# Kernel tuning notes

Hardware: AMD Instinct MI355X
Metric: run time of the kernel (lower is better)

The kernel has to match this reference:

```python
import jax, jax.numpy as jnp
import numpy as np

N, E, DIN, DH, DOUT, G, H = 40000, 400000, 256, 128, 128, 256, 4
BN_EPS = 1e-5      # nn.BatchNorm1d default
SM_EPS = 1e-16     # PyG softmax eps
NEG_SLOPE = 0.2    # GATConv default negative_slope


def _gat(x, src, dst, W, a_src, a_dst, b, heads, out_ch):
    # x:[N,Fin] W:[Fin,heads*out_ch] a_*:[heads,out_ch] b:[out_ch]
    n = x.shape[0]
    h = (x @ W).reshape(n, heads, out_ch)                     # [N,H,C]
    e = (h * a_src).sum(-1)[src] + (h * a_dst).sum(-1)[dst]   # [E,H] attention logits
    e = jnp.where(e > 0, e, NEG_SLOPE * e)                    # leaky_relu
    m = jax.ops.segment_max(e, dst, num_segments=n)           # segment softmax over incoming edges
    p = jnp.exp(e - m[dst])
    z = jax.ops.segment_sum(p, dst, num_segments=n)
    alpha = p / (z[dst] + SM_EPS)                             # [E,H]
    out = jax.ops.segment_sum(h[src] * alpha[:, :, None], dst, num_segments=n)  # [N,H,C]
    return out.mean(axis=1) + b                               # concat=False -> mean over heads, then bias


def _bn(x, g, b, m, v):
    # eval-mode BatchNorm1d with running stats
    return (x - m) * jax.lax.rsqrt(v + BN_EPS) * g + b


def setup_inputs():
    key = jax.random.key(0)
    ks = jax.random.split(key, 16)
    def rn(k, shape, fan):
        return jax.random.normal(k, shape, jnp.float32) / np.sqrt(fan).astype(np.float32)
    return {
        "x": jax.random.normal(ks[0], (N, DIN), jnp.float32),
        "src": jax.random.randint(ks[1], (E,), 0, N),
        "dst": jax.random.randint(ks[2], (E,), 0, N),
        "batch": jnp.sort(jax.random.randint(ks[3], (N,), 0, G)),
        "W1": rn(ks[4], (DIN, H * DH), DIN), "as1": rn(ks[5], (H, DH), DH), "ad1": rn(ks[6], (H, DH), DH), "b1": jnp.zeros((DH,), jnp.float32),
        "g1": jnp.ones((DH,), jnp.float32), "be1": jnp.zeros((DH,), jnp.float32), "m1": jnp.zeros((DH,), jnp.float32), "v1": jnp.ones((DH,), jnp.float32),
        "W2": rn(ks[7], (DH, H * DH), DH), "as2": rn(ks[8], (H, DH), DH), "ad2": rn(ks[9], (H, DH), DH), "b2": jnp.zeros((DH,), jnp.float32),
        "g2": jnp.ones((DH,), jnp.float32), "be2": jnp.zeros((DH,), jnp.float32), "m2": jnp.zeros((DH,), jnp.float32), "v2": jnp.ones((DH,), jnp.float32),
        "W3": rn(ks[10], (DH, DOUT), DH), "as3": rn(ks[11], (1, DOUT), DOUT), "ad3": rn(ks[12], (1, DOUT), DOUT), "b3": jnp.zeros((DOUT,), jnp.float32),
    }


def reference(x, src, dst, batch, W1, as1, ad1, b1, g1, be1, m1, v1,
              W2, as2, ad2, b2, g2, be2, m2, v2, W3, as3, ad3, b3):
    n = x.shape[0]
    loop = jnp.arange(n)
    s = jnp.concatenate([src, loop])  # PyG GATConv add_self_loops=True
    d = jnp.concatenate([dst, loop])
    h = jax.nn.elu(_gat(x, s, d, W1, as1, ad1, b1, H, DH))
    h = _bn(h, g1, be1, m1, v1)
    h = jax.nn.elu(_gat(h, s, d, W2, as2, ad2, b2, H, DH))
    h = _bn(h, g2, be2, m2, v2)
    h = _gat(h, s, d, W3, as3, ad3, b3, 1, DOUT)
    tot = jax.ops.segment_sum(h, batch, num_segments=G)      # global_mean_pool
    cnt = jax.ops.segment_sum(jnp.ones((n,), h.dtype), batch, num_segments=G)
    return tot / jnp.maximum(cnt, 1.0)[:, None]
```

## Files before the change

kernel.cpp:

```cpp
#include <hip/hip_runtime.h>
#include <cstdint>

#define N_NODES 40000
#define N_EDGES 400000
#define DIN 256
#define DHID 128
#define NG 256
#define NHEAD 4
#define ETOT (N_EDGES + N_NODES)

typedef __attribute__((ext_vector_type(8))) short short8;
typedef __attribute__((ext_vector_type(8))) unsigned short bfx8;
typedef __attribute__((ext_vector_type(4))) unsigned short bfx4;
typedef __attribute__((ext_vector_type(4))) float floatx4;

static __device__ __forceinline__ unsigned short f2bf(float f) {
    unsigned u = __float_as_uint(f);
    unsigned r = (u + 0x7FFFu + ((u >> 16) & 1u)) >> 16;
    return (unsigned short)r;
}
static __device__ __forceinline__ float bf2f(unsigned short s) {
    return __uint_as_float((unsigned)s << 16);
}


__global__ void count_kernel(const int* __restrict__ dst, int* __restrict__ deg) {
    int i = blockIdx.x * 256 + threadIdx.x;
    if (i >= ETOT) return;
    int d = (i < N_EDGES) ? dst[i] : (i - N_EDGES);
    atomicAdd(&deg[d], 1);
}

__global__ __launch_bounds__(1024) void scan_kernel(const int* __restrict__ deg,
                                                    int* __restrict__ offs,
                                                    int* __restrict__ cursor) {
    const int VPT = 40;
    __shared__ int wsum[16];
    int t = threadIdx.x;
    int lane = t & 63, wv = t >> 6;
    int base = t * VPT;
    int vals[VPT];
    int run = 0;
#pragma unroll
    for (int i = 0; i < VPT; i++) {
        int idx = base + i;
        int v = (idx < N_NODES) ? deg[idx] : 0;
        vals[i] = run;
        run += v;
    }
    int inc = run;
#pragma unroll
    for (int off = 1; off < 64; off <<= 1) {
        int n = __shfl_up(inc, off, 64);
        if (lane >= off) inc += n;
    }
    if (lane == 63) wsum[wv] = inc;
    __syncthreads();
    if (t == 0) {
        int c = 0;
#pragma unroll
        for (int i = 0; i < 16; i++) { int v = wsum[i]; wsum[i] = c; c += v; }
    }
    __syncthreads();
    int excl = wsum[wv] + inc - run;
#pragma unroll
    for (int i = 0; i < VPT; i++) {
        int idx = base + i;
        if (idx < N_NODES) { int o = excl + vals[i]; offs[idx] = o; cursor[idx] = o; }
    }
    if (t == 0) offs[N_NODES] = ETOT;
}

__global__ void fill_kernel(const int* __restrict__ src, const int* __restrict__ dst,
                            int* __restrict__ cursor, int* __restrict__ csr,
                            int* __restrict__ dstp) {
    int i = blockIdx.x * 256 + threadIdx.x;
    if (i >= ETOT) return;
    int s, d;
    if (i < N_EDGES) { s = src[i]; d = dst[i]; } else { s = d = i - N_EDGES; }
    int pos = atomicAdd(&cursor[d], 1);
    csr[pos] = s;
    dstp[pos] = d;
}


__global__ void cvt_bf16_kernel(const float* __restrict__ in, unsigned short* __restrict__ out,
                                int n) {
    int i = blockIdx.x * 256 + threadIdx.x;
    if (i >= n) return;
    out[i] = f2bf(in[i]);
}

__global__ void transpose_w_kernel(const float* __restrict__ W, unsigned short* __restrict__ Wt,
                                   int K, int Nn) {
    int i = blockIdx.x * 256 + threadIdx.x;
    if (i >= K * Nn) return;
    int k = i / Nn, n = i - k * Nn;
    Wt[(size_t)n * K + k] = f2bf(W[i]);
}


template <int K, int NCOL>
__global__ __launch_bounds__(256) void mfma_gemm_kernel(const unsigned short* __restrict__ A,
                                                        const unsigned short* __restrict__ Bt,
                                                        unsigned short* __restrict__ C,
                                                        const float* __restrict__ asrc,
                                                        const float* __restrict__ adst,
                                                        float* __restrict__ ssrc,
                                                        float* __restrict__ sdst) {
    constexpr int KC = 128;
    constexpr int KP = KC + 8;
    constexpr int SH = NCOL / 128;
    __shared__ alignas(16) unsigned short A_lds[64][KP];
    __shared__ alignas(16) unsigned short B_lds[128][KP];

    const int tid = threadIdx.x;
    const int lane = tid & 63, wave = tid >> 6;
    const int row0 = blockIdx.x * 64;
    const int head = blockIdx.y;
    const int col0 = head * 128;
    const int cq = lane & 15, rq = lane >> 4;

    floatx4 acc[4][2] = {};

    for (int k0 = 0; k0 < K; k0 += KC) {
        if (k0) __syncthreads();
#pragma unroll
        for (int r = 0; r < 4; r++) {
            int i = r * 256 + tid;
            int row = i >> 4, slot = i & 15;
            short8 v = *(const short8*)(A + (size_t)(row0 + row) * K + k0 + slot * 8);
            *(short8*)&A_lds[row][slot * 8] = v;
        }
#pragma unroll
        for (int r = 0; r < 8; r++) {
            int i = r * 256 + tid;
            int col = i >> 4, slot = i & 15;
            short8 v = *(const short8*)(Bt + (size_t)(col0 + col) * K + k0 + slot * 8);
            *(short8*)&B_lds[col][slot * 8] = v;
        }
        __syncthreads();

#pragma unroll
        for (int kk = 0; kk < KC; kk += 32) {
            short8 af[4], bfr[2];
#pragma unroll
            for (int i = 0; i < 4; i++)
                af[i] = *(const short8*)&A_lds[i * 16 + cq][kk + rq * 8];
#pragma unroll
            for (int j = 0; j < 2; j++)
                bfr[j] = *(const short8*)&B_lds[wave * 32 + j * 16 + cq][kk + rq * 8];
#pragma unroll
            for (int i = 0; i < 4; i++)
#pragma unroll
                for (int j = 0; j < 2; j++)
                    acc[i][j] = __builtin_amdgcn_mfma_f32_16x16x32_bf16(af[i], bfr[j], acc[i][j], 0, 0, 0);
        }
    }

#pragma unroll
    for (int i = 0; i < 4; i++)
#pragma unroll
        for (int j = 0; j < 2; j++) {
            unsigned short* cp = C + (size_t)(row0 + i * 16 + rq * 4) * NCOL + col0 + wave * 32 + j * 16 + cq;
#pragma unroll
            for (int r = 0; r < 4; r++)
                cp[(size_t)r * NCOL] = f2bf(acc[i][j][r]);
        }

    const float* ah = asrc + head * 128;
    const float* dh = adst + head * 128;
    float a0 = ah[wave * 32 + cq], a1 = ah[wave * 32 + 16 + cq];
    float d0 = dh[wave * 32 + cq], d1 = dh[wave * 32 + 16 + cq];

    __syncthreads();
    float* sred = (float*)&A_lds[0][0];
    float* dred = sred + 256;

#pragma unroll
    for (int i = 0; i < 4; i++)
#pragma unroll
        for (int r = 0; r < 4; r++) {
            float ss = acc[i][0][r] * a0 + acc[i][1][r] * a1;
            float sd = acc[i][0][r] * d0 + acc[i][1][r] * d1;
#pragma unroll
            for (int m = 1; m <= 8; m <<= 1) {
                ss += __shfl_xor(ss, m, 64);
                sd += __shfl_xor(sd, m, 64);
            }
            if (cq == 0) {
                int row = i * 16 + rq * 4 + r;
                sred[wave * 64 + row] = ss;
                dred[wave * 64 + row] = sd;
            }
        }
    __syncthreads();
    if (tid < 64) {
        float ss = sred[tid] + sred[64 + tid] + sred[128 + tid] + sred[192 + tid];
        float sd = dred[tid] + dred[64 + tid] + dred[128 + tid] + dred[192 + tid];
        ssrc[(size_t)(row0 + tid) * SH + head] = ss;
        sdst[(size_t)(row0 + tid) * SH + head] = sd;
    }
}


__global__ void edge_alpha4_kernel(const int* __restrict__ csr, const int* __restrict__ dstp,
                                   const float4* __restrict__ ssrc4,
                                   const float4* __restrict__ sdst4,
                                   float4* __restrict__ elog4) {
    int p = blockIdx.x * 256 + threadIdx.x;
    if (p >= ETOT) return;
    int s = csr[p], d = dstp[p];
    float4 es = ssrc4[s], ed = sdst4[d];
    float4 e;
    e.x = es.x + ed.x; e.x = e.x > 0.f ? e.x : 0.2f * e.x;
    e.y = es.y + ed.y; e.y = e.y > 0.f ? e.y : 0.2f * e.y;
    e.z = es.z + ed.z; e.z = e.z > 0.f ? e.z : 0.2f * e.z;
    e.w = es.w + ed.w; e.w = e.w > 0.f ? e.w : 0.2f * e.w;
    elog4[p] = e;
}

__global__ void edge_alpha1_kernel(const int* __restrict__ csr, const int* __restrict__ dstp,
                                   const float* __restrict__ ssrc1,
                                   const float* __restrict__ sdst1,
                                   float* __restrict__ elog1) {
    int p = blockIdx.x * 256 + threadIdx.x;
    if (p >= ETOT) return;
    int s = csr[p], d = dstp[p];
    float e = ssrc1[s] + sdst1[d];
    e = e > 0.f ? e : 0.2f * e;
    elog1[p] = e;
}


__global__ __launch_bounds__(256) void agg4_kernel(const int* __restrict__ offs,
                                                   const int* __restrict__ csr,
                                                   const unsigned short* __restrict__ hbuf,
                                                   const float4* __restrict__ elog4,
                                                   const float* __restrict__ bias,
                                                   const float* __restrict__ bng,
                                                   const float* __restrict__ bnb,
                                                   const float* __restrict__ bnm,
                                                   const float* __restrict__ bnv,
                                                   unsigned short* __restrict__ outb) {
    int wave = threadIdx.x >> 6, lane = threadIdx.x & 63;
    int d = blockIdx.x * 4 + wave;
    int off = offs[d];
    int deg = offs[d + 1] - off;
    int hh = lane >> 4;
    float acc[8] = {};

    if (deg <= 64) {
        float4 ev; int sreg = 0;
        if (lane < deg) { ev = elog4[off + lane]; sreg = csr[off + lane]; }
        else { ev.x = ev.y = ev.z = ev.w = -1e30f; }
        float4 mx = ev;
#pragma unroll
        for (int m = 32; m >= 1; m >>= 1) {
            mx.x = fmaxf(mx.x, __shfl_xor(mx.x, m, 64));
            mx.y = fmaxf(mx.y, __shfl_xor(mx.y, m, 64));
            mx.z = fmaxf(mx.z, __shfl_xor(mx.z, m, 64));
            mx.w = fmaxf(mx.w, __shfl_xor(mx.w, m, 64));
        }
        float4 p;
        p.x = (lane < deg) ? __expf(ev.x - mx.x) : 0.f;
        p.y = (lane < deg) ? __expf(ev.y - mx.y) : 0.f;
        p.z = (lane < deg) ? __expf(ev.z - mx.z) : 0.f;
        p.w = (lane < deg) ? __expf(ev.w - mx.w) : 0.f;
        float4 z = p;
#pragma unroll
        for (int m = 32; m >= 1; m >>= 1) {
            z.x += __shfl_xor(z.x, m, 64);
            z.y += __shfl_xor(z.y, m, 64);
            z.z += __shfl_xor(z.z, m, 64);
            z.w += __shfl_xor(z.w, m, 64);
        }
        float4 alpha;
        alpha.x = p.x / (z.x + 1e-16f);
        alpha.y = p.y / (z.y + 1e-16f);
        alpha.z = p.z / (z.z + 1e-16f);
        alpha.w = p.w / (z.w + 1e-16f);

        for (int j = 0; j < deg; j++) {
            int s = __shfl(sreg, j, 64);
            float a0 = __shfl(alpha.x, j, 64);
            float a1 = __shfl(alpha.y, j, 64);
            float a2 = __shfl(alpha.z, j, 64);
            float a3 = __shfl(alpha.w, j, 64);
            float a = hh == 0 ? a0 : hh == 1 ? a1 : hh == 2 ? a2 : a3;
            bfx8 hv = *(const bfx8*)(hbuf + (size_t)s * 512 + lane * 8);
#pragma unroll
            for (int i = 0; i < 8; i++) acc[i] += a * bf2f(hv[i]);
        }
    } else {
        float4 mx; mx.x = mx.y = mx.z = mx.w = -1e30f;
        for (int j = lane; j < deg; j += 64) {
            float4 e = elog4[off + j];
            mx.x = fmaxf(mx.x, e.x); mx.y = fmaxf(mx.y, e.y);
            mx.z = fmaxf(mx.z, e.z); mx.w = fmaxf(mx.w, e.w);
        }
#pragma unroll
        for (int m = 32; m >= 1; m >>= 1) {
            mx.x = fmaxf(mx.x, __shfl_xor(mx.x, m, 64));
            mx.y = fmaxf(mx.y, __shfl_xor(mx.y, m, 64));
            mx.z = fmaxf(mx.z, __shfl_xor(mx.z, m, 64));
            mx.w = fmaxf(mx.w, __shfl_xor(mx.w, m, 64));
        }
        float4 z; z.x = z.y = z.z = z.w = 0.f;
        for (int j = lane; j < deg; j += 64) {
            float4 e = elog4[off + j];
            z.x += __expf(e.x - mx.x); z.y += __expf(e.y - mx.y);
            z.z += __expf(e.z - mx.z); z.w += __expf(e.w - mx.w);
        }
#pragma unroll
        for (int m = 32; m >= 1; m >>= 1) {
            z.x += __shfl_xor(z.x, m, 64);
            z.y += __shfl_xor(z.y, m, 64);
            z.z += __shfl_xor(z.z, m, 64);
            z.w += __shfl_xor(z.w, m, 64);
        }
        float4 inv;
        inv.x = 1.f / (z.x + 1e-16f); inv.y = 1.f / (z.y + 1e-16f);
        inv.z = 1.f / (z.z + 1e-16f); inv.w = 1.f / (z.w + 1e-16f);
        float mc = hh == 0 ? mx.x : hh == 1 ? mx.y : hh == 2 ? mx.z : mx.w;
        float ic = hh == 0 ? inv.x : hh == 1 ? inv.y : hh == 2 ? inv.z : inv.w;
        for (int j = 0; j < deg; j++) {
            float4 e = elog4[off + j];
            int s = csr[off + j];
            float ec = hh == 0 ? e.x : hh == 1 ? e.y : hh == 2 ? e.z : e.w;
            float a = __expf(ec - mc) * ic;
            bfx8 hv = *(const bfx8*)(hbuf + (size_t)s * 512 + lane * 8);
#pragma unroll
            for (int i = 0; i < 8; i++) acc[i] += a * bf2f(hv[i]);
        }
    }

#pragma unroll
    for (int i = 0; i < 8; i++) {
        acc[i] += __shfl_xor(acc[i], 16, 64);
        acc[i] += __shfl_xor(acc[i], 32, 64);
    }
    if (lane < 16) {
        int c0 = lane * 8;
        bfx8 o;
#pragma unroll
        for (int i = 0; i < 8; i++) {
            int c = c0 + i;
            float v = acc[i] * 0.25f + bias[c];
            v = v > 0.f ? v : (__expf(v) - 1.0f);
            float sc = bng[c] * rsqrtf(bnv[c] + 1e-5f);
            v = (v - bnm[c]) * sc + bnb[c];
            o[i] = f2bf(v);
        }
        *(bfx8*)(outb + (size_t)d * 128 + c0) = o;
    }
}


__global__ __launch_bounds__(256) void agg1_kernel(const int* __restrict__ offs,
                                                   const int* __restrict__ csr,
                                                   const unsigned short* __restrict__ hbuf1,
                                                   const float* __restrict__ elog1,
                                                   const float* __restrict__ bias,
                                                   float* __restrict__ h3out) {
    int wave = threadIdx.x >> 6, lane = threadIdx.x & 63;
    int d = blockIdx.x * 4 + wave;
    int off = offs[d];
    int deg = offs[d + 1] - off;
    int half = lane >> 5, li = lane & 31;
    float acc[4] = {};

    if (deg <= 64) {
        float ev = -1e30f; int sreg = 0;
        if (lane < deg) { ev = elog1[off + lane]; sreg = csr[off + lane]; }
        float mx = ev;
#pragma unroll
        for (int m = 32; m >= 1; m >>= 1) mx = fmaxf(mx, __shfl_xor(mx, m, 64));
        float p = (lane < deg) ? __expf(ev - mx) : 0.f;
        float z = p;
#pragma unroll
        for (int m = 32; m >= 1; m >>= 1) z += __shfl_xor(z, m, 64);
        float alpha = p / (z + 1e-16f);
        for (int j = half; j < deg; j += 2) {
            int s = __shfl(sreg, j, 64);
            float a = __shfl(alpha, j, 64);
            bfx4 hv = *(const bfx4*)(hbuf1 + (size_t)s * 128 + li * 4);
#pragma unroll
            for (int i = 0; i < 4; i++) acc[i] += a * bf2f(hv[i]);
        }
    } else {
        float mx = -1e30f;
        for (int j = lane; j < deg; j += 64) mx = fmaxf(mx, elog1[off + j]);
#pragma unroll
        for (int m = 32; m >= 1; m >>= 1) mx = fmaxf(mx, __shfl_xor(mx, m, 64));
        float z = 0.f;
        for (int j = lane; j < deg; j += 64) z += __expf(elog1[off + j] - mx);
#pragma unroll
        for (int m = 32; m >= 1; m >>= 1) z += __shfl_xor(z, m, 64);
        float inv = 1.f / (z + 1e-16f);
        for (int j = half; j < deg; j += 2) {
            int s = csr[off + j];
            float a = __expf(elog1[off + j] - mx) * inv;
            bfx4 hv = *(const bfx4*)(hbuf1 + (size_t)s * 128 + li * 4);
#pragma unroll
            for (int i = 0; i < 4; i++) acc[i] += a * bf2f(hv[i]);
        }
    }

#pragma unroll
    for (int i = 0; i < 4; i++) acc[i] += __shfl_xor(acc[i], 32, 64);
    if (lane < 32) {
        float4 o;
        o.x = acc[0] + bias[li * 4];
        o.y = acc[1] + bias[li * 4 + 1];
        o.z = acc[2] + bias[li * 4 + 2];
        o.w = acc[3] + bias[li * 4 + 3];
        *(float4*)(h3out + (size_t)d * 128 + li * 4) = o;
    }
}


__global__ __launch_bounds__(256) void pool_kernel(const float* __restrict__ h3,
                                                   const int* __restrict__ batch,
                                                   float* __restrict__ out) {
    __shared__ float red[256];
    int g = blockIdx.x;
    int t = threadIdx.x;
    int lo = 0, n = N_NODES;
    while (n > 0) { int s = n >> 1; if (batch[lo + s] < g) { lo += s + 1; n -= s + 1; } else n = s; }
    int hi = lo; n = N_NODES - lo;
    while (n > 0) { int s = n >> 1; if (batch[hi + s] < g + 1) { hi += s + 1; n -= s + 1; } else n = s; }
    int c = t & 127;
    float acc = 0.f;
    for (int r = lo + (t >> 7); r < hi; r += 2)
        acc += h3[(size_t)r * 128 + c];
    red[t] = acc;
    __syncthreads();
    if (t < 128)
        out[(size_t)g * 128 + t] = (red[t] + red[t + 128]) / fmaxf((float)(hi - lo), 1.0f);
}


extern "C" void kernel_launch(void* const* d_in, const int* in_sizes, int n_in,
                              void* d_out, int out_size, void* d_ws, size_t ws_size,
                              hipStream_t stream) {
    const float* x    = (const float*)d_in[0];
    const int* src    = (const int*)d_in[1];
    const int* dst    = (const int*)d_in[2];
    const int* batch  = (const int*)d_in[3];
    const float* W1   = (const float*)d_in[4];
    const float* as1  = (const float*)d_in[5];
    const float* ad1  = (const float*)d_in[6];
    const float* b1   = (const float*)d_in[7];
    const float* g1   = (const float*)d_in[8];
    const float* be1  = (const float*)d_in[9];
    const float* m1   = (const float*)d_in[10];
    const float* v1   = (const float*)d_in[11];
    const float* W2   = (const float*)d_in[12];
    const float* as2  = (const float*)d_in[13];
    const float* ad2  = (const float*)d_in[14];
    const float* b2   = (const float*)d_in[15];
    const float* g2   = (const float*)d_in[16];
    const float* be2  = (const float*)d_in[17];
    const float* m2   = (const float*)d_in[18];
    const float* v2   = (const float*)d_in[19];
    const float* W3   = (const float*)d_in[20];
    const float* as3  = (const float*)d_in[21];
    const float* ad3  = (const float*)d_in[22];
    const float* b3   = (const float*)d_in[23];
    float* out = (float*)d_out;

    char* w = (char*)d_ws;
    size_t o = 0;
    auto alloc = [&](size_t bytes) -> void* {
        void* p = w + o;
        o += (bytes + 255) & ~(size_t)255;
        return p;
    };
    int* deg     = (int*)alloc((size_t)N_NODES * 4);
    int* offs    = (int*)alloc((size_t)(N_NODES + 1) * 4);
    int* cursor  = (int*)alloc((size_t)N_NODES * 4);
    int* csr     = (int*)alloc((size_t)ETOT * 4);
    int* dstp    = (int*)alloc((size_t)ETOT * 4);
    float* ssrc  = (float*)alloc((size_t)N_NODES * NHEAD * 4);
    float* sdst  = (float*)alloc((size_t)N_NODES * NHEAD * 4);
    float* elog  = (float*)alloc((size_t)ETOT * NHEAD * 4);
    float* h3out = (float*)alloc((size_t)N_NODES * 128 * 4);
    unsigned short* hbuf = (unsigned short*)alloc((size_t)N_NODES * 512 * 2);
    unsigned short* xb   = (unsigned short*)alloc((size_t)N_NODES * DIN * 2);
    unsigned short* xbuf = (unsigned short*)alloc((size_t)N_NODES * 128 * 2);
    unsigned short* W1t  = (unsigned short*)alloc((size_t)512 * 256 * 2);
    unsigned short* W2t  = (unsigned short*)alloc((size_t)512 * 128 * 2);
    unsigned short* W3t  = (unsigned short*)alloc((size_t)128 * 128 * 2);

    (void)hipMemsetAsync(deg, 0, (size_t)N_NODES * 4, stream);

    count_kernel<<<(ETOT + 255) / 256, 256, 0, stream>>>(dst, deg);
    scan_kernel<<<1, 1024, 0, stream>>>(deg, offs, cursor);
    fill_kernel<<<(ETOT + 255) / 256, 256, 0, stream>>>(src, dst, cursor, csr, dstp);

    cvt_bf16_kernel<<<(N_NODES * DIN + 255) / 256, 256, 0, stream>>>(x, xb, N_NODES * DIN);
    transpose_w_kernel<<<(256 * 512 + 255) / 256, 256, 0, stream>>>(W1, W1t, 256, 512);
    transpose_w_kernel<<<(128 * 512 + 255) / 256, 256, 0, stream>>>(W2, W2t, 128, 512);
    transpose_w_kernel<<<(128 * 128 + 255) / 256, 256, 0, stream>>>(W3, W3t, 128, 128);

    mfma_gemm_kernel<256, 512><<<dim3(N_NODES / 64, 4), 256, 0, stream>>>(
        xb, W1t, hbuf, as1, ad1, ssrc, sdst);
    edge_alpha4_kernel<<<(ETOT + 255) / 256, 256, 0, stream>>>(
        csr, dstp, (const float4*)ssrc, (const float4*)sdst, (float4*)elog);
    agg4_kernel<<<N_NODES / 4, 256, 0, stream>>>(offs, csr, hbuf, (const float4*)elog,
                                                 b1, g1, be1, m1, v1, xbuf);

    mfma_gemm_kernel<128, 512><<<dim3(N_NODES / 64, 4), 256, 0, stream>>>(
        xbuf, W2t, hbuf, as2, ad2, ssrc, sdst);
    edge_alpha4_kernel<<<(ETOT + 255) / 256, 256, 0, stream>>>(
        csr, dstp, (const float4*)ssrc, (const float4*)sdst, (float4*)elog);
    agg4_kernel<<<N_NODES / 4, 256, 0, stream>>>(offs, csr, hbuf, (const float4*)elog,
                                                 b2, g2, be2, m2, v2, xbuf);

    mfma_gemm_kernel<128, 128><<<dim3(N_NODES / 64, 1), 256, 0, stream>>>(
        xbuf, W3t, hbuf, as3, ad3, ssrc, sdst);
    edge_alpha1_kernel<<<(ETOT + 255) / 256, 256, 0, stream>>>(csr, dstp, ssrc, sdst, elog);
    agg1_kernel<<<N_NODES / 4, 256, 0, stream>>>(offs, csr, hbuf, elog, b3, h3out);

    pool_kernel<<<NG, 256, 0, stream>>>(h3out, batch, out);
}
```

Measured before the change: 518.5 us.

## Fuse edge logits into aggregation, fold bf16 input cast into GEMM, split edges across waves

Removes the separate edge-logit kernels and the dstp/elog buffers by computing leaky-relu logits inside the aggregation kernels from per-node scores. Folds the fp32-to-bf16 conversion of x into the first GEMM's A-tile load, dropping a full pass over x. The 4-head aggregation now uses two waves per node, each handling alternate edges with unrolled gathers via LDS, then combines through shared memory. This also adds more parallelism per node and more memory-level parallelism, at the cost of an LDS round-trip and a block barrier.

```diff
diff --git a/kernel.cpp b/kernel.cpp
--- a/kernel.cpp
+++ b/kernel.cpp
@@ -72,24 +72,15 @@
 }
 
 __global__ void fill_kernel(const int* __restrict__ src, const int* __restrict__ dst,
-                            int* __restrict__ cursor, int* __restrict__ csr,
-                            int* __restrict__ dstp) {
+                            int* __restrict__ cursor, int* __restrict__ csr) {
     int i = blockIdx.x * 256 + threadIdx.x;
     if (i >= ETOT) return;
     int s, d;
     if (i < N_EDGES) { s = src[i]; d = dst[i]; } else { s = d = i - N_EDGES; }
     int pos = atomicAdd(&cursor[d], 1);
     csr[pos] = s;
-    dstp[pos] = d;
-}
-
-
-__global__ void cvt_bf16_kernel(const float* __restrict__ in, unsigned short* __restrict__ out,
-                                int n) {
-    int i = blockIdx.x * 256 + threadIdx.x;
-    if (i >= n) return;
-    out[i] = f2bf(in[i]);
-}
+}
+
 
 __global__ void transpose_w_kernel(const float* __restrict__ W, unsigned short* __restrict__ Wt,
                                    int K, int Nn) {
@@ -100,8 +91,8 @@
 }
 
 
-template <int K, int NCOL>
-__global__ __launch_bounds__(256) void mfma_gemm_kernel(const unsigned short* __restrict__ A,
+template <int K, int NCOL, bool AF32>
+__global__ __launch_bounds__(256) void mfma_gemm_kernel(const void* __restrict__ Aptr,
                                                         const unsigned short* __restrict__ Bt,
                                                         unsigned short* __restrict__ C,
                                                         const float* __restrict__ asrc,
@@ -129,8 +120,20 @@
         for (int r = 0; r < 4; r++) {
             int i = r * 256 + tid;
             int row = i >> 4, slot = i & 15;
-            short8 v = *(const short8*)(A + (size_t)(row0 + row) * K + k0 + slot * 8);
-            *(short8*)&A_lds[row][slot * 8] = v;
+            if constexpr (AF32) {
+                const float* ap = (const float*)Aptr + (size_t)(row0 + row) * K + k0 + slot * 8;
+                float4 u0 = *(const float4*)ap;
+                float4 u1 = *(const float4*)(ap + 4);
+                short8 v;
+                v[0] = (short)f2bf(u0.x); v[1] = (short)f2bf(u0.y);
+                v[2] = (short)f2bf(u0.z); v[3] = (short)f2bf(u0.w);
+                v[4] = (short)f2bf(u1.x); v[5] = (short)f2bf(u1.y);
+                v[6] = (short)f2bf(u1.z); v[7] = (short)f2bf(u1.w);
+                *(short8*)&A_lds[row][slot * 8] = v;
+            } else {
+                const unsigned short* ap = (const unsigned short*)Aptr + (size_t)(row0 + row) * K + k0 + slot * 8;
+                *(short8*)&A_lds[row][slot * 8] = *(const short8*)ap;
+            }
         }
 #pragma unroll
         for (int r = 0; r < 8; r++) {
@@ -204,56 +207,41 @@
 }
 
 
-__global__ void edge_alpha4_kernel(const int* __restrict__ csr, const int* __restrict__ dstp,
-                                   const float4* __restrict__ ssrc4,
-                                   const float4* __restrict__ sdst4,
-                                   float4* __restrict__ elog4) {
-    int p = blockIdx.x * 256 + threadIdx.x;
-    if (p >= ETOT) return;
-    int s = csr[p], d = dstp[p];
-    float4 es = ssrc4[s], ed = sdst4[d];
-    float4 e;
-    e.x = es.x + ed.x; e.x = e.x > 0.f ? e.x : 0.2f * e.x;
-    e.y = es.y + ed.y; e.y = e.y > 0.f ? e.y : 0.2f * e.y;
-    e.z = es.z + ed.z; e.z = e.z > 0.f ? e.z : 0.2f * e.z;
-    e.w = es.w + ed.w; e.w = e.w > 0.f ? e.w : 0.2f * e.w;
-    elog4[p] = e;
-}
-
-__global__ void edge_alpha1_kernel(const int* __restrict__ csr, const int* __restrict__ dstp,
-                                   const float* __restrict__ ssrc1,
-                                   const float* __restrict__ sdst1,
-                                   float* __restrict__ elog1) {
-    int p = blockIdx.x * 256 + threadIdx.x;
-    if (p >= ETOT) return;
-    int s = csr[p], d = dstp[p];
-    float e = ssrc1[s] + sdst1[d];
-    e = e > 0.f ? e : 0.2f * e;
-    elog1[p] = e;
-}
-
-
 __global__ __launch_bounds__(256) void agg4_kernel(const int* __restrict__ offs,
                                                    const int* __restrict__ csr,
                                                    const unsigned short* __restrict__ hbuf,
-                                                   const float4* __restrict__ elog4,
+                                                   const float4* __restrict__ ssrc4,
+                                                   const float4* __restrict__ sdst4,
                                                    const float* __restrict__ bias,
                                                    const float* __restrict__ bng,
                                                    const float* __restrict__ bnb,
                                                    const float* __restrict__ bnm,
                                                    const float* __restrict__ bnv,
                                                    unsigned short* __restrict__ outb) {
+    __shared__ alignas(16) float aload[4][64][4];
+    __shared__ int sload[4][64];
+    __shared__ float red[2][128];
+
     int wave = threadIdx.x >> 6, lane = threadIdx.x & 63;
-    int d = blockIdx.x * 4 + wave;
+    int nodeb = wave >> 1, w2 = wave & 1;
+    int d = blockIdx.x * 2 + nodeb;
     int off = offs[d];
     int deg = offs[d + 1] - off;
     int hh = lane >> 4;
+    float4 sdv = sdst4[d];
     float acc[8] = {};
 
     if (deg <= 64) {
-        float4 ev; int sreg = 0;
-        if (lane < deg) { ev = elog4[off + lane]; sreg = csr[off + lane]; }
-        else { ev.x = ev.y = ev.z = ev.w = -1e30f; }
+        int sreg = 0;
+        float4 ev;
+        if (lane < deg) {
+            sreg = csr[off + lane];
+            float4 es = ssrc4[sreg];
+            ev.x = es.x + sdv.x; ev.x = ev.x > 0.f ? ev.x : 0.2f * ev.x;
+            ev.y = es.y + sdv.y; ev.y = ev.y > 0.f ? ev.y : 0.2f * ev.y;
+            ev.z = es.z + sdv.z; ev.z = ev.z > 0.f ? ev.z : 0.2f * ev.z;
+            ev.w = es.w + sdv.w; ev.w = ev.w > 0.f ? ev.w : 0.2f * ev.w;
+        } else { ev.x = ev.y = ev.z = ev.w = -1e30f; }
         float4 mx = ev;
 #pragma unroll
         for (int m = 32; m >= 1; m >>= 1) {
@@ -281,13 +269,27 @@
         alpha.z = p.z / (z.z + 1e-16f);
         alpha.w = p.w / (z.w + 1e-16f);
 
-        for (int j = 0; j < deg; j++) {
-            int s = __shfl(sreg, j, 64);
-            float a0 = __shfl(alpha.x, j, 64);
-            float a1 = __shfl(alpha.y, j, 64);
-            float a2 = __shfl(alpha.z, j, 64);
-            float a3 = __shfl(alpha.w, j, 64);
-            float a = hh == 0 ? a0 : hh == 1 ? a1 : hh == 2 ? a2 : a3;
+        *(float4*)&aload[wave][lane][0] = alpha;
+        sload[wave][lane] = sreg;
+
+        int j = w2;
+        for (; j + 6 < deg; j += 8) {
+            int s0 = sload[wave][j],     s1 = sload[wave][j + 2];
+            int s2 = sload[wave][j + 4], s3 = sload[wave][j + 6];
+            float a0 = aload[wave][j][hh],     a1 = aload[wave][j + 2][hh];
+            float a2 = aload[wave][j + 4][hh], a3 = aload[wave][j + 6][hh];
+            bfx8 v0 = *(const bfx8*)(hbuf + (size_t)s0 * 512 + lane * 8);
+            bfx8 v1 = *(const bfx8*)(hbuf + (size_t)s1 * 512 + lane * 8);
+            bfx8 v2 = *(const bfx8*)(hbuf + (size_t)s2 * 512 + lane * 8);
+            bfx8 v3 = *(const bfx8*)(hbuf + (size_t)s3 * 512 + lane * 8);
+#pragma unroll
+            for (int i = 0; i < 8; i++)
+                acc[i] += a0 * bf2f(v0[i]) + a1 * bf2f(v1[i]) +
+                          a2 * bf2f(v2[i]) + a3 * bf2f(v3[i]);
+        }
+        for (; j < deg; j += 2) {
+            int s = sload[wave][j];
+            float a = aload[wave][j][hh];
             bfx8 hv = *(const bfx8*)(hbuf + (size_t)s * 512 + lane * 8);
 #pragma unroll
             for (int i = 0; i < 8; i++) acc[i] += a * bf2f(hv[i]);
@@ -295,7 +297,13 @@
     } else {
         float4 mx; mx.x = mx.y = mx.z = mx.w = -1e30f;
         for (int j = lane; j < deg; j += 64) {
-            float4 e = elog4[off + j];
+            int s = csr[off + j];
+            float4 es = ssrc4[s];
+            float4 e;
+            e.x = es.x + sdv.x; e.x = e.x > 0.f ? e.x : 0.2f * e.x;
+            e.y = es.y + sdv.y; e.y = e.y > 0.f ? e.y : 0.2f * e.y;
+            e.z = es.z + sdv.z; e.z = e.z > 0.f ? e.z : 0.2f * e.z;
+            e.w = es.w + sdv.w; e.w = e.w > 0.f ? e.w : 0.2f * e.w;
             mx.x = fmaxf(mx.x, e.x); mx.y = fmaxf(mx.y, e.y);
             mx.z = fmaxf(mx.z, e.z); mx.w = fmaxf(mx.w, e.w);
         }
@@ -308,7 +316,13 @@
         }
         float4 z; z.x = z.y = z.z = z.w = 0.f;
         for (int j = lane; j < deg; j += 64) {
-            float4 e = elog4[off + j];
+            int s = csr[off + j];
+            float4 es = ssrc4[s];
+            float4 e;
+            e.x = es.x + sdv.x; e.x = e.x > 0.f ? e.x : 0.2f * e.x;
+            e.y = es.y + sdv.y; e.y = e.y > 0.f ? e.y : 0.2f * e.y;
+            e.z = es.z + sdv.z; e.z = e.z > 0.f ? e.z : 0.2f * e.z;
+            e.w = es.w + sdv.w; e.w = e.w > 0.f ? e.w : 0.2f * e.w;
             z.x += __expf(e.x - mx.x); z.y += __expf(e.y - mx.y);
             z.z += __expf(e.z - mx.z); z.w += __expf(e.w - mx.w);
         }
@@ -319,15 +333,15 @@
             z.z += __shfl_xor(z.z, m, 64);
             z.w += __shfl_xor(z.w, m, 64);
         }
-        float4 inv;
-        inv.x = 1.f / (z.x + 1e-16f); inv.y = 1.f / (z.y + 1e-16f);
-        inv.z = 1.f / (z.z + 1e-16f); inv.w = 1.f / (z.w + 1e-16f);
         float mc = hh == 0 ? mx.x : hh == 1 ? mx.y : hh == 2 ? mx.z : mx.w;
-        float ic = hh == 0 ? inv.x : hh == 1 ? inv.y : hh == 2 ? inv.z : inv.w;
-        for (int j = 0; j < deg; j++) {
-            float4 e = elog4[off + j];
+        float zc = hh == 0 ? z.x : hh == 1 ? z.y : hh == 2 ? z.z : z.w;
+        float ic = 1.f / (zc + 1e-16f);
+        float sdc = hh == 0 ? sdv.x : hh == 1 ? sdv.y : hh == 2 ? sdv.z : sdv.w;
+        for (int j = w2; j < deg; j += 2) {
             int s = csr[off + j];
-            float ec = hh == 0 ? e.x : hh == 1 ? e.y : hh == 2 ? e.z : e.w;
+            float4 es = ssrc4[s];
+            float ec = hh == 0 ? es.x : hh == 1 ? es.y : hh == 2 ? es.z : es.w;
+            ec += sdc; ec = ec > 0.f ? ec : 0.2f * ec;
             float a = __expf(ec - mc) * ic;
             bfx8 hv = *(const bfx8*)(hbuf + (size_t)s * 512 + lane * 8);
 #pragma unroll
@@ -340,13 +354,18 @@
         acc[i] += __shfl_xor(acc[i], 16, 64);
         acc[i] += __shfl_xor(acc[i], 32, 64);
     }
-    if (lane < 16) {
+    if (w2 == 0 && lane < 16) {
+#pragma unroll
+        for (int i = 0; i < 8; i++) red[nodeb][lane * 8 + i] = acc[i];
+    }
+    __syncthreads();
+    if (w2 == 1 && lane < 16) {
         int c0 = lane * 8;
         bfx8 o;
 #pragma unroll
         for (int i = 0; i < 8; i++) {
             int c = c0 + i;
-            float v = acc[i] * 0.25f + bias[c];
+            float v = (red[nodeb][c] + acc[i]) * 0.25f + bias[c];
             v = v > 0.f ? v : (__expf(v) - 1.0f);
             float sc = bng[c] * rsqrtf(bnv[c] + 1e-5f);
             v = (v - bnm[c]) * sc + bnb[c];
@@ -360,19 +379,27 @@
 __global__ __launch_bounds__(256) void agg1_kernel(const int* __restrict__ offs,
                                                    const int* __restrict__ csr,
                                                    const unsigned short* __restrict__ hbuf1,
-                                                   const float* __restrict__ elog1,
+                                                   const float* __restrict__ ssrc1,
+                                                   const float* __restrict__ sdst1,
                                                    const float* __restrict__ bias,
                                                    float* __restrict__ h3out) {
+    __shared__ float aload[4][64];
+    __shared__ int sload[4][64];
     int wave = threadIdx.x >> 6, lane = threadIdx.x & 63;
     int d = blockIdx.x * 4 + wave;
     int off = offs[d];
     int deg = offs[d + 1] - off;
     int half = lane >> 5, li = lane & 31;
+    float sdv = sdst1[d];
     float acc[4] = {};
 
     if (deg <= 64) {
         float ev = -1e30f; int sreg = 0;
-        if (lane < deg) { ev = elog1[off + lane]; sreg = csr[off + lane]; }
+        if (lane < deg) {
+            sreg = csr[off + lane];
+            ev = ssrc1[sreg] + sdv;
+            ev = ev > 0.f ? ev : 0.2f * ev;
+        }
         float mx = ev;
 #pragma unroll
         for (int m = 32; m >= 1; m >>= 1) mx = fmaxf(mx, __shfl_xor(mx, m, 64));
@@ -380,27 +407,49 @@
         float z = p;
 #pragma unroll
         for (int m = 32; m >= 1; m >>= 1) z += __shfl_xor(z, m, 64);
-        float alpha = p / (z + 1e-16f);
-        for (int j = half; j < deg; j += 2) {
-            int s = __shfl(sreg, j, 64);
-            float a = __shfl(alpha, j, 64);
+        aload[wave][lane] = p / (z + 1e-16f);
+        sload[wave][lane] = sreg;
+
+        int j = half;
+        for (; j + 2 < deg; j += 4) {
+            int s0 = sload[wave][j], s1 = sload[wave][j + 2];
+            float a0 = aload[wave][j], a1 = aload[wave][j + 2];
+            bfx4 v0 = *(const bfx4*)(hbuf1 + (size_t)s0 * 128 + li * 4);
+            bfx4 v1 = *(const bfx4*)(hbuf1 + (size_t)s1 * 128 + li * 4);
+#pragma unroll
+            for (int i = 0; i < 4; i++)
+                acc[i] += a0 * bf2f(v0[i]) + a1 * bf2f(v1[i]);
+        }
+        for (; j < deg; j += 2) {
+            int s = sload[wave][j];
+            float a = aload[wave][j];
             bfx4 hv = *(const bfx4*)(hbuf1 + (size_t)s * 128 + li * 4);
 #pragma unroll
             for (int i = 0; i < 4; i++) acc[i] += a * bf2f(hv[i]);
         }
     } else {
         float mx = -1e30f;
-        for (int j = lane; j < deg; j += 64) mx = fmaxf(mx, elog1[off + j]);
+        for (int j = lane; j < deg; j += 64) {
+            float e = ssrc1[csr[off + j]] + sdv;
+            e = e > 0.f ? e : 0.2f * e;
+            mx = fmaxf(mx, e);
+        }
 #pragma unroll
         for (int m = 32; m >= 1; m >>= 1) mx = fmaxf(mx, __shfl_xor(mx, m, 64));
         float z = 0.f;
-        for (int j = lane; j < deg; j += 64) z += __expf(elog1[off + j] - mx);
+        for (int j = lane; j < deg; j += 64) {
+            float e = ssrc1[csr[off + j]] + sdv;
+            e = e > 0.f ? e : 0.2f * e;
+            z += __expf(e - mx);
+        }
 #pragma unroll
         for (int m = 32; m >= 1; m >>= 1) z += __shfl_xor(z, m, 64);
         float inv = 1.f / (z + 1e-16f);
         for (int j = half; j < deg; j += 2) {
             int s = csr[off + j];
-            float a = __expf(elog1[off + j] - mx) * inv;
+            float e = ssrc1[s] + sdv;
+            e = e > 0.f ? e : 0.2f * e;
+            float a = __expf(e - mx) * inv;
             bfx4 hv = *(const bfx4*)(hbuf1 + (size_t)s * 128 + li * 4);
 #pragma unroll
             for (int i = 0; i < 4; i++) acc[i] += a * bf2f(hv[i]);
@@ -481,13 +530,10 @@
     int* offs    = (int*)alloc((size_t)(N_NODES + 1) * 4);
     int* cursor  = (int*)alloc((size_t)N_NODES * 4);
     int* csr     = (int*)alloc((size_t)ETOT * 4);
-    int* dstp    = (int*)alloc((size_t)ETOT * 4);
     float* ssrc  = (float*)alloc((size_t)N_NODES * NHEAD * 4);
     float* sdst  = (float*)alloc((size_t)N_NODES * NHEAD * 4);
-    float* elog  = (float*)alloc((size_t)ETOT * NHEAD * 4);
     float* h3out = (float*)alloc((size_t)N_NODES * 128 * 4);
     unsigned short* hbuf = (unsigned short*)alloc((size_t)N_NODES * 512 * 2);
-    unsigned short* xb   = (unsigned short*)alloc((size_t)N_NODES * DIN * 2);
     unsigned short* xbuf = (unsigned short*)alloc((size_t)N_NODES * 128 * 2);
     unsigned short* W1t  = (unsigned short*)alloc((size_t)512 * 256 * 2);
     unsigned short* W2t  = (unsigned short*)alloc((size_t)512 * 128 * 2);
@@ -497,31 +543,25 @@
 
     count_kernel<<<(ETOT + 255) / 256, 256, 0, stream>>>(dst, deg);
     scan_kernel<<<1, 1024, 0, stream>>>(deg, offs, cursor);
-    fill_kernel<<<(ETOT + 255) / 256, 256, 0, stream>>>(src, dst, cursor, csr, dstp);
-
-    cvt_bf16_kernel<<<(N_NODES * DIN + 255) / 256, 256, 0, stream>>>(x, xb, N_NODES * DIN);
+    fill_kernel<<<(ETOT + 255) / 256, 256, 0, stream>>>(src, dst, cursor, csr);
+
     transpose_w_kernel<<<(256 * 512 + 255) / 256, 256, 0, stream>>>(W1, W1t, 256, 512);
     transpose_w_kernel<<<(128 * 512 + 255) / 256, 256, 0, stream>>>(W2, W2t, 128, 512);
     transpose_w_kernel<<<(128 * 128 + 255) / 256, 256, 0, stream>>>(W3, W3t, 128, 128);
 
-    mfma_gemm_kernel<256, 512><<<dim3(N_NODES / 64, 4), 256, 0, stream>>>(
-        xb, W1t, hbuf, as1, ad1, ssrc, sdst);
-    edge_alpha4_kernel<<<(ETOT + 255) / 256, 256, 0, stream>>>(
-        csr, dstp, (const float4*)ssrc, (const float4*)sdst, (float4*)elog);
-    agg4_kernel<<<N_NODES / 4, 256, 0, stream>>>(offs, csr, hbuf, (const float4*)elog,
-                                                 b1, g1, be1, m1, v1, xbuf);
-
-    mfma_gemm_kernel<128, 512><<<dim3(N_NODES / 64, 4), 256, 0, stream>>>(
+    mfma_gemm_kernel<256, 512, true><<<dim3(N_NODES / 64, 4), 256, 0, stream>>>(
+        x, W1t, hbuf, as1, ad1, ssrc, sdst);
+    agg4_kernel<<<N_NODES / 2, 256, 0, stream>>>(offs, csr, hbuf, (const float4*)ssrc,
+                                                 (const float4*)sdst, b1, g1, be1, m1, v1, xbuf);
+
+    mfma_gemm_kernel<128, 512, false><<<dim3(N_NODES / 64, 4), 256, 0, stream>>>(
         xbuf, W2t, hbuf, as2, ad2, ssrc, sdst);
-    edge_alpha4_kernel<<<(ETOT + 255) / 256, 256, 0, stream>>>(
-        csr, dstp, (const float4*)ssrc, (const float4*)sdst, (float4*)elog);
-    agg4_kernel<<<N_NODES / 4, 256, 0, stream>>>(offs, csr, hbuf, (const float4*)elog,
-                                                 b2, g2, be2, m2, v2, xbuf);
-
-    mfma_gemm_kernel<128, 128><<<dim3(N_NODES / 64, 1), 256, 0, stream>>>(
+    agg4_kernel<<<N_NODES / 2, 256, 0, stream>>>(offs, csr, hbuf, (const float4*)ssrc,
+                                                 (const float4*)sdst, b2, g2, be2, m2, v2, xbuf);
+
+    mfma_gemm_kernel<128, 128, false><<<dim3(N_NODES / 64, 1), 256, 0, stream>>>(
         xbuf, W3t, hbuf, as3, ad3, ssrc, sdst);
-    edge_alpha1_kernel<<<(ETOT + 255) / 256, 256, 0, stream>>>(csr, dstp, ssrc, sdst, elog);
-    agg1_kernel<<<N_NODES / 4, 256, 0, stream>>>(offs, csr, hbuf, elog, b3, h3out);
+    agg1_kernel<<<N_NODES / 4, 256, 0, stream>>>(offs, csr, hbuf, ssrc, sdst, b3, h3out);
 
     pool_kernel<<<NG, 256, 0, stream>>>(h3out, batch, out);
 }
```

After: 503.7 us. 1.03x faster.
